# Optimization experiments

Hardware: AMD Instinct MI355X
Metric: run time of the kernel (lower is better)

## Reference

```python
import jax, jax.numpy as jnp
import numpy as np

HORIZON = 8


def _gru_pass(seq, h0, w_ih, w_hh, b_ih, b_hh):
    """Run a single-layer PyTorch-convention GRU over seq (batch_first) starting
    from hidden h0; return the final hidden state (== out[:, -1, :]).
    seq: [B, T, I], h0: [B, H], w_ih: [3H, I], w_hh: [3H, H].
    Gate order (PyTorch): r, z, n."""
    # Precompute input projections for all timesteps: [B, T, 3H] -> [T, B, 3H]
    x_proj = jnp.einsum('bti,gi->btg', seq, w_ih) + b_ih
    x_proj = jnp.swapaxes(x_proj, 0, 1)

    def step(h, xp):
        hp = h @ w_hh.T + b_hh                      # [B, 3H]
        xr, xz, xn = jnp.split(xp, 3, axis=-1)
        hr, hz, hn = jnp.split(hp, 3, axis=-1)
        r = jax.nn.sigmoid(xr + hr)
        z = jax.nn.sigmoid(xz + hz)
        n = jnp.tanh(xn + r * hn)
        h_new = (1.0 - z) * n + z * h
        return h_new, None

    h_final, _ = jax.lax.scan(step, h0, x_proj)
    return h_final


def setup_inputs() -> dict:
    key = jax.random.key(0)
    ks = jax.random.split(key, 7)
    B, T, I, H = 256, 256, 64, 512
    scale = 0.04  # ~1/sqrt(H), matches PyTorch uniform init magnitude
    return {
        'x': jax.random.normal(ks[0], (B, T, I), dtype=jnp.float32),
        'w_ih': jax.random.normal(ks[1], (3 * H, I), dtype=jnp.float32) * scale,
        'w_hh': jax.random.normal(ks[2], (3 * H, H), dtype=jnp.float32) * scale,
        'b_ih': jax.random.normal(ks[3], (3 * H,), dtype=jnp.float32) * scale,
        'b_hh': jax.random.normal(ks[4], (3 * H,), dtype=jnp.float32) * scale,
        'fc_w': jax.random.normal(ks[5], (I, H), dtype=jnp.float32) * scale,
        'fc_b': jax.random.normal(ks[6], (I,), dtype=jnp.float32) * scale,
    }


def reference(x, w_ih, w_hh, b_ih, b_hh, fc_w, fc_b):
    """Faithful translation of PredictorRNN.forward: each horizon step re-runs
    the GRU over the whole growing sequence, carrying hidden state h between
    passes (matching the original torch code's out,h = rnn(seq, h))."""
    B = x.shape[0]
    H = w_hh.shape[1]
    h = jnp.zeros((B, H), dtype=x.dtype)  # h=None -> zeros in torch
    seq = x
    preds = []
    for _ in range(HORIZON):
        h = _gru_pass(seq, h, w_ih, w_hh, b_ih, b_hh)  # == out[:, -1, :]
        step = h @ fc_w.T + fc_b                       # [B, I]
        preds.append(step)
        seq = jnp.concatenate([seq, step[:, None, :]], axis=1)
    return jnp.stack(preds, axis=1)  # [B, horizon, I]
```

## Files before the change

### kernel.cpp

```cpp
#include <hip/hip_runtime.h>


typedef __attribute__((ext_vector_type(8))) short short8;
typedef __attribute__((ext_vector_type(4))) float floatx4;

#define B_    256
#define T_    256
#define I_    64
#define H_    512
#define HZ    8
#define LPAD  520
#define HLSZ  (16 * LPAD)

#define MFMA_BF16(acc, a, b) \
  acc = __builtin_amdgcn_mfma_f32_16x16x32_bf16((a), (b), (acc), 0, 0, 0)

#define POLL_BACKOFF(it)                         \
  do {                                           \
    if ((it) < 2)      __builtin_amdgcn_s_sleep(1);  \
    else if ((it) < 8) __builtin_amdgcn_s_sleep(4);  \
    else               __builtin_amdgcn_s_sleep(16); \
  } while (0)

__device__ __forceinline__ float bf2f(unsigned short u) {
  union { unsigned int i; float f; } v; v.i = ((unsigned int)u) << 16; return v.f;
}
__device__ __forceinline__ unsigned short f2bf(float f) {
  union { float f; unsigned int i; } v; v.f = f;
  return (unsigned short)((v.i + 0x7FFFu + ((v.i >> 16) & 1u)) >> 16);
}
__device__ __forceinline__ short8 ld8_f32_to_bf16(const float* p) {
  short8 r;
#pragma unroll
  for (int e = 0; e < 8; ++e) r[e] = (short)f2bf(p[e]);
  return r;
}
__device__ __forceinline__ float sigm(float xx) {
  return __builtin_amdgcn_rcpf(1.f + __expf(-xx));
}
__device__ __forceinline__ float tanh_fast(float xx) {
  float e = __expf(2.f * xx);
  return 1.f - 2.f * __builtin_amdgcn_rcpf(e + 1.f);
}
__device__ __forceinline__ unsigned long long ald64(const unsigned int* p) {
  return __hip_atomic_load((const unsigned long long*)p, __ATOMIC_RELAXED,
                           __HIP_MEMORY_SCOPE_AGENT);
}
__device__ __forceinline__ void ast32(unsigned int* p, unsigned int v) {
  __hip_atomic_store(p, v, __ATOMIC_RELAXED, __HIP_MEMORY_SCOPE_AGENT);
}

extern "C" __global__ void __launch_bounds__(256, 1)
gru_chain(const float* __restrict__ x,
          const float* __restrict__ w_ih,
          const float* __restrict__ w_hh,
          const float* __restrict__ b_ih,
          const float* __restrict__ b_hh,
          const float* __restrict__ fc_w,
          const float* __restrict__ fc_b,
          float* __restrict__ out,
          unsigned int* __restrict__ hbuf,
          unsigned int* __restrict__ xext)
{
  const int tid  = threadIdx.x;
  const int wave = tid >> 6;
  const int lane = tid & 63;
  const int bx   = blockIdx.x;
  const int grp  = bx & 15;
  const int ju   = ((bx >> 4) << 2) | wave;
  const int n16  = lane & 15;
  const int quad = lane >> 4;
  const int jg   = ju * 16 + n16;
  const int rowbase = grp * 16;

  __shared__ __align__(16) unsigned short hls[2 * HLSZ];

  short8 wR[18], wZ[18], wHN[16], wXN[2];
  {
    const int koff = quad * 8;
    const float* whr = w_hh + (size_t)(0 * H_ + jg) * H_ + koff;
    const float* whz = w_hh + (size_t)(1 * H_ + jg) * H_ + koff;
    const float* whn = w_hh + (size_t)(2 * H_ + jg) * H_ + koff;
#pragma unroll
    for (int kc = 0; kc < 16; ++kc) {
      wR[kc]  = ld8_f32_to_bf16(whr + kc * 32);
      wZ[kc]  = ld8_f32_to_bf16(whz + kc * 32);
      wHN[kc] = ld8_f32_to_bf16(whn + kc * 32);
    }
    const float* wir = w_ih + (size_t)(0 * H_ + jg) * I_ + koff;
    const float* wiz = w_ih + (size_t)(1 * H_ + jg) * I_ + koff;
    const float* win = w_ih + (size_t)(2 * H_ + jg) * I_ + koff;
#pragma unroll
    for (int kc = 0; kc < 2; ++kc) {
      wR[16 + kc] = ld8_f32_to_bf16(wir + kc * 32);
      wZ[16 + kc] = ld8_f32_to_bf16(wiz + kc * 32);
      wXN[kc]     = ld8_f32_to_bf16(win + kc * 32);
    }
  }
  const float brc = b_ih[jg]          + b_hh[jg];
  const float bzc = b_ih[H_ + jg]     + b_hh[H_ + jg];
  const float bxn = b_ih[2 * H_ + jg];
  const float bhn = b_hh[2 * H_ + jg];

  float hloc[4] = {0.f, 0.f, 0.f, 0.f};

  int s = 0;
  for (int p = 0; p < HZ; ++p) {
    const int Tp = T_ + p;
    for (int t = 0; t < Tp; ++t) {
      short8 xaf0, xaf1;
      if (t < T_) {
        const float* xs = x + ((size_t)(rowbase + n16) * T_ + t) * I_ + quad * 8;
        xaf0 = ld8_f32_to_bf16(xs);
        xaf1 = ld8_f32_to_bf16(xs + 32);
      }
      unsigned short* hl = &hls[(s & 1) * HLSZ];
      if (s > 0) {
        const unsigned int want = (unsigned int)s;
        const unsigned int* hb = hbuf + (size_t)((s + 1) & 1) * (B_ * H_) +
                                 (size_t)rowbase * H_;
        unsigned long long v[16];
#pragma unroll
        for (int i = 0; i < 16; ++i) {
          int c = tid + (i << 8), r = c >> 8, o = (c & 255) << 1;
          v[i] = ald64(hb + (size_t)r * H_ + o);
        }
        int it = 0;
        for (;;) {
          bool all = true;
#pragma unroll
          for (int i = 0; i < 16; ++i) {
            unsigned int w0 = (unsigned int)v[i];
            unsigned int w1 = (unsigned int)(v[i] >> 32);
            if (((w0 >> 16) != want) || ((w1 >> 16) != want)) {
              all = false;
              int c = tid + (i << 8), r = c >> 8, o = (c & 255) << 1;
              v[i] = ald64(hb + (size_t)r * H_ + o);
            }
          }
          if (all) break;
          POLL_BACKOFF(it);
          ++it;
        }
#pragma unroll
        for (int i = 0; i < 16; ++i) {
          int c = tid + (i << 8), r = c >> 8, o = (c & 255) << 1;
          unsigned int w0 = (unsigned int)v[i];
          unsigned int w1 = (unsigned int)(v[i] >> 32);
          *(unsigned int*)&hl[r * LPAD + o] = (w0 & 0xffffu) | (w1 << 16);
        }
      } else {
#pragma unroll
        for (int i = 0; i < 16; ++i) {
          int c = tid + (i << 8), r = c >> 8, o = (c & 255) << 1;
          *(unsigned int*)&hl[r * LPAD + o] = 0u;
        }
      }
      if (t >= T_) {
        const int p2 = t - T_;
        const unsigned int wantx = (unsigned int)(p2 + 1);
        const unsigned int* xb =
            xext + ((size_t)p2 * B_ + rowbase + n16) * I_;
        unsigned long long u[8];
#pragma unroll
        for (int k = 0; k < 8; ++k) {
          int off = (k < 4) ? (quad * 8 + 2 * k) : (32 + quad * 8 + 2 * (k - 4));
          u[k] = ald64(xb + off);
        }
        int it = 0;
        for (;;) {
          bool all = true;
#pragma unroll
          for (int k = 0; k < 8; ++k) {
            unsigned int w0 = (unsigned int)u[k];
            unsigned int w1 = (unsigned int)(u[k] >> 32);
            if (((w0 >> 16) != wantx) || ((w1 >> 16) != wantx)) {
              all = false;
              int off = (k < 4) ? (quad * 8 + 2 * k)
                                : (32 + quad * 8 + 2 * (k - 4));
              u[k] = ald64(xb + off);
            }
          }
          if (all) break;
          POLL_BACKOFF(it);
          ++it;
        }
#pragma unroll
        for (int k = 0; k < 4; ++k) {
          xaf0[2 * k]     = (short)(unsigned short)u[k];
          xaf0[2 * k + 1] = (short)(unsigned short)(u[k] >> 32);
          xaf1[2 * k]     = (short)(unsigned short)u[4 + k];
          xaf1[2 * k + 1] = (short)(unsigned short)(u[4 + k] >> 32);
        }
      }
      __syncthreads();
      short8 haf[16];
#pragma unroll
      for (int kc = 0; kc < 16; ++kc)
        haf[kc] = *(const short8*)&hl[n16 * LPAD + kc * 32 + quad * 8];

      floatx4 aR = {0.f, 0.f, 0.f, 0.f};
      floatx4 aZ = {0.f, 0.f, 0.f, 0.f};
      floatx4 aN = {0.f, 0.f, 0.f, 0.f};
      floatx4 aX = {0.f, 0.f, 0.f, 0.f};
#pragma unroll
      for (int kc = 0; kc < 16; ++kc) {
        MFMA_BF16(aR, haf[kc], wR[kc]);
        MFMA_BF16(aZ, haf[kc], wZ[kc]);
        MFMA_BF16(aN, haf[kc], wHN[kc]);
      }
      MFMA_BF16(aR, xaf0, wR[16]);  MFMA_BF16(aR, xaf1, wR[17]);
      MFMA_BF16(aZ, xaf0, wZ[16]);  MFMA_BF16(aZ, xaf1, wZ[17]);
      MFMA_BF16(aX, xaf0, wXN[0]);  MFMA_BF16(aX, xaf1, wXN[1]);

      unsigned int* hd = hbuf + (size_t)(s & 1) * (B_ * H_);
      const unsigned int tg = ((unsigned int)(s + 1)) << 16;
#pragma unroll
      for (int i = 0; i < 4; ++i) {
        float rv = sigm(aR[i] + brc);
        float zv = sigm(aZ[i] + bzc);
        float nv = tanh_fast(aX[i] + bxn + rv * (aN[i] + bhn));
        float hn = (1.f - zv) * nv + zv * hloc[i];
        hloc[i]  = hn;
        ast32(&hd[(size_t)(rowbase + quad * 4 + i) * H_ + jg],
              tg | (unsigned int)f2bf(hn));
      }
      ++s;
    }
    {
      unsigned short* hl = &hls[(s & 1) * HLSZ];
      const unsigned int want = (unsigned int)s;
      const unsigned int* hb = hbuf + (size_t)((s + 1) & 1) * (B_ * H_) +
                               (size_t)rowbase * H_;
      unsigned long long v[16];
#pragma unroll
      for (int i = 0; i < 16; ++i) {
        int c = tid + (i << 8), r = c >> 8, o = (c & 255) << 1;
        v[i] = ald64(hb + (size_t)r * H_ + o);
      }
      int it = 0;
      for (;;) {
        bool all = true;
#pragma unroll
        for (int i = 0; i < 16; ++i) {
          unsigned int w0 = (unsigned int)v[i];
          unsigned int w1 = (unsigned int)(v[i] >> 32);
          if (((w0 >> 16) != want) || ((w1 >> 16) != want)) {
            all = false;
            int c = tid + (i << 8), r = c >> 8, o = (c & 255) << 1;
            v[i] = ald64(hb + (size_t)r * H_ + o);
          }
        }
        if (all) break;
        POLL_BACKOFF(it);
        ++it;
      }
#pragma unroll
      for (int i = 0; i < 16; ++i) {
        int c = tid + (i << 8), r = c >> 8, o = (c & 255) << 1;
        unsigned int w0 = (unsigned int)v[i];
        unsigned int w1 = (unsigned int)(v[i] >> 32);
        *(unsigned int*)&hl[r * LPAD + o] = (w0 & 0xffffu) | (w1 << 16);
      }
      __syncthreads();
      const int mm  = lane & 15;
      const int sub = lane >> 4;
#pragma unroll
      for (int cc = 0; cc < 2; ++cc) {
        const int c = ju * 2 + cc;
        const unsigned short* hrow = &hl[mm * LPAD + sub * 128];
        const float* wrow = fc_w + (size_t)c * H_ + sub * 128;
        float acc = 0.f;
#pragma unroll
        for (int kk = 0; kk < 128; kk += 8) {
          short8 hv = *(const short8*)(hrow + kk);
#pragma unroll
          for (int e = 0; e < 8; ++e)
            acc = fmaf(bf2f((unsigned short)hv[e]), wrow[kk + e], acc);
        }
        acc += __shfl_xor(acc, 16, 64);
        acc += __shfl_xor(acc, 32, 64);
        if (sub == 0) {
          float val = acc + fc_b[c];
          out[((size_t)(rowbase + mm) * HZ + p) * I_ + c] = val;
          ast32(&xext[((size_t)p * B_ + rowbase + mm) * I_ + c],
                (((unsigned int)(p + 1)) << 16) | (unsigned int)f2bf(val));
        }
      }
      __syncthreads();
    }
  }
}

extern "C" void kernel_launch(void* const* d_in, const int* in_sizes, int n_in,
                              void* d_out, int out_size, void* d_ws, size_t ws_size,
                              hipStream_t stream) {
  const float* x    = (const float*)d_in[0];
  const float* w_ih = (const float*)d_in[1];
  const float* w_hh = (const float*)d_in[2];
  const float* b_ih = (const float*)d_in[3];
  const float* b_hh = (const float*)d_in[4];
  const float* fc_w = (const float*)d_in[5];
  const float* fc_b = (const float*)d_in[6];
  float* out = (float*)d_out;

  unsigned char* ws = (unsigned char*)d_ws;
  const size_t hbuf_b = (size_t)2 * B_ * H_ * 4;
  const size_t xext_b = (size_t)HZ * B_ * I_ * 4;
  unsigned int* hbuf = (unsigned int*)ws;
  unsigned int* xext = (unsigned int*)(ws + hbuf_b);

  hipMemsetAsync(d_ws, 0, hbuf_b + xext_b, stream);

  gru_chain<<<dim3(128), dim3(256), 0, stream>>>(
      x, w_ih, w_hh, b_ih, b_hh, fc_w, fc_b, out, hbuf, xext);
}
```

Measured before the change: 6.456 ms.

## Co-locate each batch group on one XCD and sync through L2-scope polling

At launch, each block reads its XCD id and takes a ticket from a per-XCD counter. If every XCD holds exactly 16 blocks, blocks are remapped so that all 8 blocks sharing a batch-row group run on the same XCD; a handshake confirms the mapping, and otherwise the old blockIdx mapping is kept. With the co-located mapping, hidden-state and feedback exchanges use workgroup-scope stores, sc0 loads with explicit vmcnt fences, and a shorter backoff schedule. The aim is to keep per-timestep cross-block synchronisation inside one XCD's L2 instead of going through agent-scope coherence across XCDs, at the cost of an extra startup handshake and reliance on hardware block placement and memory-scope behaviour.

```diff
diff --git a/kernel.cpp b/kernel.cpp
--- a/kernel.cpp
+++ b/kernel.cpp
@@ -15,12 +15,26 @@
 #define MFMA_BF16(acc, a, b) \
   acc = __builtin_amdgcn_mfma_f32_16x16x32_bf16((a), (b), (acc), 0, 0, 0)
 
-#define POLL_BACKOFF(it)                         \
+#define POLL_BACKOFF_MALL(it)                    \
   do {                                           \
     if ((it) < 2)      __builtin_amdgcn_s_sleep(1);  \
     else if ((it) < 8) __builtin_amdgcn_s_sleep(4);  \
     else               __builtin_amdgcn_s_sleep(16); \
   } while (0)
+#define POLL_BACKOFF_L2(it)                      \
+  do {                                           \
+    if ((it) < 4)       __builtin_amdgcn_s_sleep(1); \
+    else if ((it) < 12) __builtin_amdgcn_s_sleep(2); \
+    else                __builtin_amdgcn_s_sleep(8); \
+  } while (0)
+
+#define LD64_SC0(dst, addr) \
+  asm volatile("global_load_dwordx2 %0, %1, off sc0" : "=v"(dst) : "v"(addr))
+#define VM_FENCE()                                       \
+  do {                                                   \
+    asm volatile("s_waitcnt vmcnt(0)" ::: "memory");     \
+    __builtin_amdgcn_sched_barrier(0);                   \
+  } while (0)
 
 __device__ __forceinline__ float bf2f(unsigned short u) {
   union { unsigned int i; float f; } v; v.i = ((unsigned int)u) << 16; return v.f;
@@ -46,8 +60,235 @@
   return __hip_atomic_load((const unsigned long long*)p, __ATOMIC_RELAXED,
                            __HIP_MEMORY_SCOPE_AGENT);
 }
+__device__ __forceinline__ unsigned int ald32(const unsigned int* p) {
+  return __hip_atomic_load(p, __ATOMIC_RELAXED, __HIP_MEMORY_SCOPE_AGENT);
+}
 __device__ __forceinline__ void ast32(unsigned int* p, unsigned int v) {
   __hip_atomic_store(p, v, __ATOMIC_RELAXED, __HIP_MEMORY_SCOPE_AGENT);
+}
+__device__ __forceinline__ void st32_wg(unsigned int* p, unsigned int v) {
+  __hip_atomic_store(p, v, __ATOMIC_RELAXED, __HIP_MEMORY_SCOPE_WORKGROUP);
+}
+
+template <bool PURE>
+__device__ __forceinline__ void stage_h16(unsigned short* hl,
+                                          const unsigned int* hb,
+                                          unsigned int want, int tid) {
+  unsigned long long v[16];
+#pragma unroll
+  for (int i = 0; i < 16; ++i) {
+    int c = tid + (i << 8), r = c >> 8, o = (c & 255) << 1;
+    if constexpr (PURE) { LD64_SC0(v[i], hb + (size_t)r * H_ + o); }
+    else                { v[i] = ald64(hb + (size_t)r * H_ + o); }
+  }
+  if constexpr (PURE) VM_FENCE();
+  int it = 0;
+  for (;;) {
+    bool all = true;
+#pragma unroll
+    for (int i = 0; i < 16; ++i) {
+      unsigned int w0 = (unsigned int)v[i];
+      unsigned int w1 = (unsigned int)(v[i] >> 32);
+      if (((w0 >> 16) != want) || ((w1 >> 16) != want)) {
+        all = false;
+        int c = tid + (i << 8), r = c >> 8, o = (c & 255) << 1;
+        if constexpr (PURE) { LD64_SC0(v[i], hb + (size_t)r * H_ + o); }
+        else                { v[i] = ald64(hb + (size_t)r * H_ + o); }
+      }
+    }
+    if (all) break;
+    if constexpr (PURE) POLL_BACKOFF_L2(it); else POLL_BACKOFF_MALL(it);
+    ++it;
+    if constexpr (PURE) VM_FENCE();
+  }
+#pragma unroll
+  for (int i = 0; i < 16; ++i) {
+    int c = tid + (i << 8), r = c >> 8, o = (c & 255) << 1;
+    unsigned int w0 = (unsigned int)v[i];
+    unsigned int w1 = (unsigned int)(v[i] >> 32);
+    *(unsigned int*)&hl[r * LPAD + o] = (w0 & 0xffffu) | (w1 << 16);
+  }
+}
+
+template <bool PURE>
+__device__ __forceinline__ void body(
+    const float* __restrict__ x, const float* __restrict__ w_ih,
+    const float* __restrict__ w_hh, const float* __restrict__ b_ih,
+    const float* __restrict__ b_hh, const float* __restrict__ fc_w,
+    const float* __restrict__ fc_b, float* __restrict__ out,
+    unsigned int* __restrict__ hbuf, unsigned int* __restrict__ xext,
+    unsigned short* hls, int grp, int slot) {
+  const int tid  = threadIdx.x;
+  const int wave = tid >> 6;
+  const int lane = tid & 63;
+  const int ju   = (slot << 2) | wave;
+  const int n16  = lane & 15;
+  const int quad = lane >> 4;
+  const int jg   = ju * 16 + n16;
+  const int rowbase = grp * 16;
+
+  short8 wR[18], wZ[18], wHN[16], wXN[2];
+  {
+    const int koff = quad * 8;
+    const float* whr = w_hh + (size_t)(0 * H_ + jg) * H_ + koff;
+    const float* whz = w_hh + (size_t)(1 * H_ + jg) * H_ + koff;
+    const float* whn = w_hh + (size_t)(2 * H_ + jg) * H_ + koff;
+#pragma unroll
+    for (int kc = 0; kc < 16; ++kc) {
+      wR[kc]  = ld8_f32_to_bf16(whr + kc * 32);
+      wZ[kc]  = ld8_f32_to_bf16(whz + kc * 32);
+      wHN[kc] = ld8_f32_to_bf16(whn + kc * 32);
+    }
+    const float* wir = w_ih + (size_t)(0 * H_ + jg) * I_ + koff;
+    const float* wiz = w_ih + (size_t)(1 * H_ + jg) * I_ + koff;
+    const float* win = w_ih + (size_t)(2 * H_ + jg) * I_ + koff;
+#pragma unroll
+    for (int kc = 0; kc < 2; ++kc) {
+      wR[16 + kc] = ld8_f32_to_bf16(wir + kc * 32);
+      wZ[16 + kc] = ld8_f32_to_bf16(wiz + kc * 32);
+      wXN[kc]     = ld8_f32_to_bf16(win + kc * 32);
+    }
+  }
+  const float brc = b_ih[jg]          + b_hh[jg];
+  const float bzc = b_ih[H_ + jg]     + b_hh[H_ + jg];
+  const float bxn = b_ih[2 * H_ + jg];
+  const float bhn = b_hh[2 * H_ + jg];
+
+  float hloc[4] = {0.f, 0.f, 0.f, 0.f};
+
+  int s = 0;
+  for (int p = 0; p < HZ; ++p) {
+    const int Tp = T_ + p;
+    for (int t = 0; t < Tp; ++t) {
+      short8 xaf0, xaf1;
+      if (t < T_) {
+        const float* xs = x + ((size_t)(rowbase + n16) * T_ + t) * I_ + quad * 8;
+        xaf0 = ld8_f32_to_bf16(xs);
+        xaf1 = ld8_f32_to_bf16(xs + 32);
+      }
+      unsigned short* hl = &hls[(s & 1) * HLSZ];
+      if (s > 0) {
+        const unsigned int* hb = hbuf + (size_t)((s + 1) & 1) * (B_ * H_) +
+                                 (size_t)rowbase * H_;
+        stage_h16<PURE>(hl, hb, (unsigned int)s, tid);
+      } else {
+#pragma unroll
+        for (int i = 0; i < 16; ++i) {
+          int c = tid + (i << 8), r = c >> 8, o = (c & 255) << 1;
+          *(unsigned int*)&hl[r * LPAD + o] = 0u;
+        }
+      }
+      if (t >= T_) {
+        const int p2 = t - T_;
+        const unsigned int wantx = (unsigned int)(p2 + 1);
+        const unsigned int* xb =
+            xext + ((size_t)p2 * B_ + rowbase + n16) * I_;
+        unsigned long long u[8];
+#pragma unroll
+        for (int k = 0; k < 8; ++k) {
+          int off = (k < 4) ? (quad * 8 + 2 * k) : (32 + quad * 8 + 2 * (k - 4));
+          if constexpr (PURE) { LD64_SC0(u[k], xb + off); }
+          else                { u[k] = ald64(xb + off); }
+        }
+        if constexpr (PURE) VM_FENCE();
+        int it = 0;
+        for (;;) {
+          bool all = true;
+#pragma unroll
+          for (int k = 0; k < 8; ++k) {
+            unsigned int w0 = (unsigned int)u[k];
+            unsigned int w1 = (unsigned int)(u[k] >> 32);
+            if (((w0 >> 16) != wantx) || ((w1 >> 16) != wantx)) {
+              all = false;
+              int off = (k < 4) ? (quad * 8 + 2 * k)
+                                : (32 + quad * 8 + 2 * (k - 4));
+              if constexpr (PURE) { LD64_SC0(u[k], xb + off); }
+              else                { u[k] = ald64(xb + off); }
+            }
+          }
+          if (all) break;
+          if constexpr (PURE) POLL_BACKOFF_L2(it); else POLL_BACKOFF_MALL(it);
+          ++it;
+          if constexpr (PURE) VM_FENCE();
+        }
+#pragma unroll
+        for (int k = 0; k < 4; ++k) {
+          xaf0[2 * k]     = (short)(unsigned short)u[k];
+          xaf0[2 * k + 1] = (short)(unsigned short)(u[k] >> 32);
+          xaf1[2 * k]     = (short)(unsigned short)u[4 + k];
+          xaf1[2 * k + 1] = (short)(unsigned short)(u[4 + k] >> 32);
+        }
+      }
+      __syncthreads();
+      short8 haf[16];
+#pragma unroll
+      for (int kc = 0; kc < 16; ++kc)
+        haf[kc] = *(const short8*)&hl[n16 * LPAD + kc * 32 + quad * 8];
+
+      floatx4 aR = {0.f, 0.f, 0.f, 0.f};
+      floatx4 aZ = {0.f, 0.f, 0.f, 0.f};
+      floatx4 aN = {0.f, 0.f, 0.f, 0.f};
+      floatx4 aX = {0.f, 0.f, 0.f, 0.f};
+#pragma unroll
+      for (int kc = 0; kc < 16; ++kc) {
+        MFMA_BF16(aR, haf[kc], wR[kc]);
+        MFMA_BF16(aZ, haf[kc], wZ[kc]);
+        MFMA_BF16(aN, haf[kc], wHN[kc]);
+      }
+      MFMA_BF16(aR, xaf0, wR[16]);  MFMA_BF16(aR, xaf1, wR[17]);
+      MFMA_BF16(aZ, xaf0, wZ[16]);  MFMA_BF16(aZ, xaf1, wZ[17]);
+      MFMA_BF16(aX, xaf0, wXN[0]);  MFMA_BF16(aX, xaf1, wXN[1]);
+
+      unsigned int* hd = hbuf + (size_t)(s & 1) * (B_ * H_);
+      const unsigned int tg = ((unsigned int)(s + 1)) << 16;
+#pragma unroll
+      for (int i = 0; i < 4; ++i) {
+        float rv = sigm(aR[i] + brc);
+        float zv = sigm(aZ[i] + bzc);
+        float nv = tanh_fast(aX[i] + bxn + rv * (aN[i] + bhn));
+        float hn = (1.f - zv) * nv + zv * hloc[i];
+        hloc[i]  = hn;
+        unsigned int* dst = &hd[(size_t)(rowbase + quad * 4 + i) * H_ + jg];
+        unsigned int val = tg | (unsigned int)f2bf(hn);
+        if constexpr (PURE) st32_wg(dst, val); else ast32(dst, val);
+      }
+      ++s;
+    }
+    {
+      unsigned short* hl = &hls[(s & 1) * HLSZ];
+      const unsigned int* hb = hbuf + (size_t)((s + 1) & 1) * (B_ * H_) +
+                               (size_t)rowbase * H_;
+      stage_h16<PURE>(hl, hb, (unsigned int)s, tid);
+      __syncthreads();
+      const int mm  = lane & 15;
+      const int sub = lane >> 4;
+#pragma unroll
+      for (int cc = 0; cc < 2; ++cc) {
+        const int c = ju * 2 + cc;
+        const unsigned short* hrow = &hl[mm * LPAD + sub * 128];
+        const float* wrow = fc_w + (size_t)c * H_ + sub * 128;
+        float acc = 0.f;
+#pragma unroll
+        for (int kk = 0; kk < 128; kk += 8) {
+          short8 hv = *(const short8*)(hrow + kk);
+#pragma unroll
+          for (int e = 0; e < 8; ++e)
+            acc = fmaf(bf2f((unsigned short)hv[e]), wrow[kk + e], acc);
+        }
+        acc += __shfl_xor(acc, 16, 64);
+        acc += __shfl_xor(acc, 32, 64);
+        if (sub == 0) {
+          float val = acc + fc_b[c];
+          out[((size_t)(rowbase + mm) * HZ + p) * I_ + c] = val;
+          unsigned int* xd = &xext[((size_t)p * B_ + rowbase + mm) * I_ + c];
+          unsigned int xv = (((unsigned int)(p + 1)) << 16) |
+                            (unsigned int)f2bf(val);
+          if constexpr (PURE) st32_wg(xd, xv); else ast32(xd, xv);
+        }
+      }
+      __syncthreads();
+    }
+  }
 }
 
 extern "C" __global__ void __launch_bounds__(256, 1)
@@ -60,236 +301,68 @@
           const float* __restrict__ fc_b,
           float* __restrict__ out,
           unsigned int* __restrict__ hbuf,
-          unsigned int* __restrict__ xext)
+          unsigned int* __restrict__ xext,
+          unsigned int* __restrict__ ctrl)
 {
-  const int tid  = threadIdx.x;
-  const int wave = tid >> 6;
-  const int lane = tid & 63;
-  const int bx   = blockIdx.x;
-  const int grp  = bx & 15;
-  const int ju   = ((bx >> 4) << 2) | wave;
-  const int n16  = lane & 15;
-  const int quad = lane >> 4;
-  const int jg   = ju * 16 + n16;
-  const int rowbase = grp * 16;
-
   __shared__ __align__(16) unsigned short hls[2 * HLSZ];
-
-  short8 wR[18], wZ[18], wHN[16], wXN[2];
-  {
-    const int koff = quad * 8;
-    const float* whr = w_hh + (size_t)(0 * H_ + jg) * H_ + koff;
-    const float* whz = w_hh + (size_t)(1 * H_ + jg) * H_ + koff;
-    const float* whn = w_hh + (size_t)(2 * H_ + jg) * H_ + koff;
-#pragma unroll
-    for (int kc = 0; kc < 16; ++kc) {
-      wR[kc]  = ld8_f32_to_bf16(whr + kc * 32);
-      wZ[kc]  = ld8_f32_to_bf16(whz + kc * 32);
-      wHN[kc] = ld8_f32_to_bf16(whn + kc * 32);
-    }
-    const float* wir = w_ih + (size_t)(0 * H_ + jg) * I_ + koff;
-    const float* wiz = w_ih + (size_t)(1 * H_ + jg) * I_ + koff;
-    const float* win = w_ih + (size_t)(2 * H_ + jg) * I_ + koff;
-#pragma unroll
-    for (int kc = 0; kc < 2; ++kc) {
-      wR[16 + kc] = ld8_f32_to_bf16(wir + kc * 32);
-      wZ[16 + kc] = ld8_f32_to_bf16(wiz + kc * 32);
-      wXN[kc]     = ld8_f32_to_bf16(win + kc * 32);
-    }
-  }
-  const float brc = b_ih[jg]          + b_hh[jg];
-  const float bzc = b_ih[H_ + jg]     + b_hh[H_ + jg];
-  const float bxn = b_ih[2 * H_ + jg];
-  const float bhn = b_hh[2 * H_ + jg];
-
-  float hloc[4] = {0.f, 0.f, 0.f, 0.f};
-
-  int s = 0;
-  for (int p = 0; p < HZ; ++p) {
-    const int Tp = T_ + p;
-    for (int t = 0; t < Tp; ++t) {
-      short8 xaf0, xaf1;
-      if (t < T_) {
-        const float* xs = x + ((size_t)(rowbase + n16) * T_ + t) * I_ + quad * 8;
-        xaf0 = ld8_f32_to_bf16(xs);
-        xaf1 = ld8_f32_to_bf16(xs + 32);
-      }
-      unsigned short* hl = &hls[(s & 1) * HLSZ];
-      if (s > 0) {
-        const unsigned int want = (unsigned int)s;
-        const unsigned int* hb = hbuf + (size_t)((s + 1) & 1) * (B_ * H_) +
-                                 (size_t)rowbase * H_;
-        unsigned long long v[16];
-#pragma unroll
-        for (int i = 0; i < 16; ++i) {
-          int c = tid + (i << 8), r = c >> 8, o = (c & 255) << 1;
-          v[i] = ald64(hb + (size_t)r * H_ + o);
-        }
-        int it = 0;
-        for (;;) {
-          bool all = true;
-#pragma unroll
-          for (int i = 0; i < 16; ++i) {
-            unsigned int w0 = (unsigned int)v[i];
-            unsigned int w1 = (unsigned int)(v[i] >> 32);
-            if (((w0 >> 16) != want) || ((w1 >> 16) != want)) {
-              all = false;
-              int c = tid + (i << 8), r = c >> 8, o = (c & 255) << 1;
-              v[i] = ald64(hb + (size_t)r * H_ + o);
-            }
-          }
-          if (all) break;
-          POLL_BACKOFF(it);
-          ++it;
-        }
-#pragma unroll
-        for (int i = 0; i < 16; ++i) {
-          int c = tid + (i << 8), r = c >> 8, o = (c & 255) << 1;
-          unsigned int w0 = (unsigned int)v[i];
-          unsigned int w1 = (unsigned int)(v[i] >> 32);
-          *(unsigned int*)&hl[r * LPAD + o] = (w0 & 0xffffu) | (w1 << 16);
-        }
-      } else {
-#pragma unroll
-        for (int i = 0; i < 16; ++i) {
-          int c = tid + (i << 8), r = c >> 8, o = (c & 255) << 1;
-          *(unsigned int*)&hl[r * LPAD + o] = 0u;
-        }
-      }
-      if (t >= T_) {
-        const int p2 = t - T_;
-        const unsigned int wantx = (unsigned int)(p2 + 1);
-        const unsigned int* xb =
-            xext + ((size_t)p2 * B_ + rowbase + n16) * I_;
-        unsigned long long u[8];
-#pragma unroll
-        for (int k = 0; k < 8; ++k) {
-          int off = (k < 4) ? (quad * 8 + 2 * k) : (32 + quad * 8 + 2 * (k - 4));
-          u[k] = ald64(xb + off);
-        }
-        int it = 0;
-        for (;;) {
-          bool all = true;
-#pragma unroll
-          for (int k = 0; k < 8; ++k) {
-            unsigned int w0 = (unsigned int)u[k];
-            unsigned int w1 = (unsigned int)(u[k] >> 32);
-            if (((w0 >> 16) != wantx) || ((w1 >> 16) != wantx)) {
-              all = false;
-              int off = (k < 4) ? (quad * 8 + 2 * k)
-                                : (32 + quad * 8 + 2 * (k - 4));
-              u[k] = ald64(xb + off);
-            }
-          }
-          if (all) break;
-          POLL_BACKOFF(it);
-          ++it;
-        }
-#pragma unroll
-        for (int k = 0; k < 4; ++k) {
-          xaf0[2 * k]     = (short)(unsigned short)u[k];
-          xaf0[2 * k + 1] = (short)(unsigned short)(u[k] >> 32);
-          xaf1[2 * k]     = (short)(unsigned short)u[4 + k];
-          xaf1[2 * k + 1] = (short)(unsigned short)(u[4 + k] >> 32);
-        }
-      }
-      __syncthreads();
-      short8 haf[16];
-#pragma unroll
-      for (int kc = 0; kc < 16; ++kc)
-        haf[kc] = *(const short8*)&hl[n16 * LPAD + kc * 32 + quad * 8];
-
-      floatx4 aR = {0.f, 0.f, 0.f, 0.f};
-      floatx4 aZ = {0.f, 0.f, 0.f, 0.f};
-      floatx4 aN = {0.f, 0.f, 0.f, 0.f};
-      floatx4 aX = {0.f, 0.f, 0.f, 0.f};
-#pragma unroll
-      for (int kc = 0; kc < 16; ++kc) {
-        MFMA_BF16(aR, haf[kc], wR[kc]);
-        MFMA_BF16(aZ, haf[kc], wZ[kc]);
-        MFMA_BF16(aN, haf[kc], wHN[kc]);
-      }
-      MFMA_BF16(aR, xaf0, wR[16]);  MFMA_BF16(aR, xaf1, wR[17]);
-      MFMA_BF16(aZ, xaf0, wZ[16]);  MFMA_BF16(aZ, xaf1, wZ[17]);
-      MFMA_BF16(aX, xaf0, wXN[0]);  MFMA_BF16(aX, xaf1, wXN[1]);
-
-      unsigned int* hd = hbuf + (size_t)(s & 1) * (B_ * H_);
-      const unsigned int tg = ((unsigned int)(s + 1)) << 16;
-#pragma unroll
-      for (int i = 0; i < 4; ++i) {
-        float rv = sigm(aR[i] + brc);
-        float zv = sigm(aZ[i] + bzc);
-        float nv = tanh_fast(aX[i] + bxn + rv * (aN[i] + bhn));
-        float hn = (1.f - zv) * nv + zv * hloc[i];
-        hloc[i]  = hn;
-        ast32(&hd[(size_t)(rowbase + quad * 4 + i) * H_ + jg],
-              tg | (unsigned int)f2bf(hn));
-      }
-      ++s;
-    }
-    {
-      unsigned short* hl = &hls[(s & 1) * HLSZ];
-      const unsigned int want = (unsigned int)s;
-      const unsigned int* hb = hbuf + (size_t)((s + 1) & 1) * (B_ * H_) +
-                               (size_t)rowbase * H_;
-      unsigned long long v[16];
-#pragma unroll
-      for (int i = 0; i < 16; ++i) {
-        int c = tid + (i << 8), r = c >> 8, o = (c & 255) << 1;
-        v[i] = ald64(hb + (size_t)r * H_ + o);
-      }
-      int it = 0;
-      for (;;) {
-        bool all = true;
-#pragma unroll
-        for (int i = 0; i < 16; ++i) {
-          unsigned int w0 = (unsigned int)v[i];
-          unsigned int w1 = (unsigned int)(v[i] >> 32);
-          if (((w0 >> 16) != want) || ((w1 >> 16) != want)) {
-            all = false;
-            int c = tid + (i << 8), r = c >> 8, o = (c & 255) << 1;
-            v[i] = ald64(hb + (size_t)r * H_ + o);
-          }
-        }
-        if (all) break;
-        POLL_BACKOFF(it);
-        ++it;
-      }
-#pragma unroll
-      for (int i = 0; i < 16; ++i) {
-        int c = tid + (i << 8), r = c >> 8, o = (c & 255) << 1;
-        unsigned int w0 = (unsigned int)v[i];
-        unsigned int w1 = (unsigned int)(v[i] >> 32);
-        *(unsigned int*)&hl[r * LPAD + o] = (w0 & 0xffffu) | (w1 << 16);
-      }
-      __syncthreads();
-      const int mm  = lane & 15;
-      const int sub = lane >> 4;
-#pragma unroll
-      for (int cc = 0; cc < 2; ++cc) {
-        const int c = ju * 2 + cc;
-        const unsigned short* hrow = &hl[mm * LPAD + sub * 128];
-        const float* wrow = fc_w + (size_t)c * H_ + sub * 128;
-        float acc = 0.f;
-#pragma unroll
-        for (int kk = 0; kk < 128; kk += 8) {
-          short8 hv = *(const short8*)(hrow + kk);
-#pragma unroll
-          for (int e = 0; e < 8; ++e)
-            acc = fmaf(bf2f((unsigned short)hv[e]), wrow[kk + e], acc);
-        }
-        acc += __shfl_xor(acc, 16, 64);
-        acc += __shfl_xor(acc, 32, 64);
-        if (sub == 0) {
-          float val = acc + fc_b[c];
-          out[((size_t)(rowbase + mm) * HZ + p) * I_ + c] = val;
-          ast32(&xext[((size_t)p * B_ + rowbase + mm) * I_ + c],
-                (((unsigned int)(p + 1)) << 16) | (unsigned int)f2bf(val));
-        }
-      }
-      __syncthreads();
-    }
-  }
+  __shared__ int s_asn;
+
+  if (threadIdx.x == 0) {
+    unsigned int xcd;
+    asm volatile("s_getreg_b32 %0, hwreg(HW_REG_XCC_ID)" : "=s"(xcd));
+    xcd &= 7u;
+    unsigned int tk = __hip_atomic_fetch_add(&ctrl[xcd], 1u, __ATOMIC_RELAXED,
+                                             __HIP_MEMORY_SCOPE_AGENT);
+    unsigned int c[8];
+    for (;;) {
+      unsigned int sum = 0;
+#pragma unroll
+      for (int i = 0; i < 8; ++i) { c[i] = ald32(&ctrl[i]); sum += c[i]; }
+      if (sum >= 128u) break;
+      __builtin_amdgcn_s_sleep(8);
+    }
+    int pure = 1;
+#pragma unroll
+    for (int i = 0; i < 8; ++i) pure &= (c[i] == 16u);
+    int grp, slot;
+    if (pure) { grp = (int)(xcd * 2u + (tk >> 3)); slot = (int)(tk & 7u); }
+    else      { grp = (int)(blockIdx.x & 15u);     slot = (int)(blockIdx.x >> 4); }
+    if (pure) {
+      unsigned int* gs = ctrl + 16;
+      st32_wg(&gs[grp * 8 + slot], 1u);
+      int ok = 1;
+      for (int k = 0; k < 8 && ok; ++k) {
+        unsigned int vv = 0;
+        for (int sp = 0; sp < 512; ++sp) {
+          asm volatile("global_load_dword %0, %1, off sc0\n\t"
+                       "s_waitcnt vmcnt(0)"
+                       : "=v"(vv) : "v"(gs + grp * 8 + k) : "memory");
+          if (vv) break;
+          __builtin_amdgcn_s_sleep(1);
+        }
+        if (!vv) ok = 0;
+      }
+      __hip_atomic_fetch_add(&ctrl[9], (unsigned int)ok, __ATOMIC_RELAXED,
+                             __HIP_MEMORY_SCOPE_AGENT);
+      __hip_atomic_fetch_add(&ctrl[10], 1u, __ATOMIC_RELAXED,
+                             __HIP_MEMORY_SCOPE_AGENT);
+      while (ald32(&ctrl[10]) < 128u) __builtin_amdgcn_s_sleep(4);
+      pure = (ald32(&ctrl[9]) == 128u) ? 1 : 0;
+      if (!pure) { grp = (int)(blockIdx.x & 15u); slot = (int)(blockIdx.x >> 4); }
+    }
+    s_asn = (grp << 5) | (slot << 1) | pure;
+  }
+  __syncthreads();
+  const int asn  = s_asn;
+  const int grp  = asn >> 5;
+  const int slot = (asn >> 1) & 15;
+
+  if (asn & 1)
+    body<true>(x, w_ih, w_hh, b_ih, b_hh, fc_w, fc_b, out, hbuf, xext,
+               hls, grp, slot);
+  else
+    body<false>(x, w_ih, w_hh, b_ih, b_hh, fc_w, fc_b, out, hbuf, xext,
+                hls, grp, slot);
 }
 
 extern "C" void kernel_launch(void* const* d_in, const int* in_sizes, int n_in,
@@ -309,9 +382,10 @@
   const size_t xext_b = (size_t)HZ * B_ * I_ * 4;
   unsigned int* hbuf = (unsigned int*)ws;
   unsigned int* xext = (unsigned int*)(ws + hbuf_b);
+  unsigned int* ctrl = xext + (size_t)(HZ - 1) * B_ * I_;
 
   hipMemsetAsync(d_ws, 0, hbuf_b + xext_b, stream);
 
   gru_chain<<<dim3(128), dim3(256), 0, stream>>>(
-      x, w_ih, w_hh, b_ih, b_hh, fc_w, fc_b, out, hbuf, xext);
-}
+      x, w_ih, w_hh, b_ih, b_hh, fc_w, fc_b, out, hbuf, xext, ctrl);
+}
```

Result: slower. 6.826 ms (+5.7%).
